# Kernel optimization log

Hardware: AMD Instinct MI355X
Metric: run time of the kernel (lower is better)

The kernel has to match this reference:

```python
import jax, jax.numpy as jnp
import numpy as np
from jax import lax

EPS = 1e-5

def binarize(x):
    # sign forward, straight-through (identity) backward, matching torch .data-trick Binarize
    return x + lax.stop_gradient(jnp.sign(x) - x)

def conv2d(x, w, pad):
    return lax.conv_general_dilated(x, w, window_strides=(1, 1),
                                    padding=[(pad, pad), (pad, pad)],
                                    dimension_numbers=('NCHW', 'OIHW', 'NCHW'))

def maxpool_k2s1(x):
    return lax.reduce_window(x, -jnp.inf, lax.max, (1, 1, 2, 2), (1, 1, 1, 1), 'VALID')

def batchnorm(x, g, b):
    # training-mode BN: batch statistics over (N, H, W)
    mean = jnp.mean(x, axis=(0, 2, 3), keepdims=True)
    var = jnp.var(x, axis=(0, 2, 3), keepdims=True)
    return (x - mean) * lax.rsqrt(var + EPS) * g[None, :, None, None] + b[None, :, None, None]

def hardtanh(x):
    return jnp.clip(x, -1.0, 1.0)

def setup_inputs() -> dict:
    key = jax.random.key(0)
    ks = jax.random.split(key, 11)
    B = 4096
    return {
        'x':   jax.random.normal(ks[0], (B, 12, 12, 15), jnp.float32),
        'w1':  jax.random.normal(ks[1], (48, 12, 3, 3), jnp.float32) * 0.1,
        'g1':  1.0 + 0.1 * jax.random.normal(ks[2], (48,), jnp.float32),
        'b1':  0.1 * jax.random.normal(ks[3], (48,), jnp.float32),
        'w2':  jax.random.normal(ks[4], (48, 48, 3, 3), jnp.float32) * 0.1,
        'g2':  1.0 + 0.1 * jax.random.normal(ks[5], (48,), jnp.float32),
        'b2':  0.1 * jax.random.normal(ks[6], (48,), jnp.float32),
        'w3':  jax.random.normal(ks[7], (48, 48, 3, 3), jnp.float32) * 0.1,
        'g3':  1.0 + 0.1 * jax.random.normal(ks[8], (48,), jnp.float32),
        'b3':  0.1 * jax.random.normal(ks[9], (48,), jnp.float32),
        'wfc': jax.random.normal(ks[10], (5, 54 * 48), jnp.float32) * 0.02,
    }

def reference(x, w1, g1, b1, w2, g2, b2, w3, g3, b3, wfc):
    # BinarizeConv2d binarizes activations (in_channels != 3) and weights; returns binarized input too
    xb1 = binarize(x)                                  # [B,12,12,15]
    h = conv2d(xb1, binarize(w1), pad=1)               # [B,48,12,15]
    h = maxpool_k2s1(h)                                # [B,48,11,14]
    h = hardtanh(batchnorm(h, g1, b1))
    xb2 = binarize(h)
    h = conv2d(xb2, binarize(w2), pad=0)               # [B,48,9,12]
    h = hardtanh(batchnorm(h, g2, b2))
    xb3 = binarize(h)
    h = conv2d(xb3, binarize(w3), pad=0)               # [B,48,7,10]
    h = maxpool_k2s1(h)                                # [B,48,6,9] -> 54 spatial
    h = hardtanh(batchnorm(h, g3, b3))
    f = h.reshape(h.shape[0], -1)                      # [B, 2592]
    fb = binarize(f)
    out = fb @ binarize(wfc).T                         # [B, 5]  (LogSoftmax defined but never applied)
    return (out, xb1, xb2, xb3, fb)
```

## Files before the change

kernel.cpp:

```cpp
#include <hip/hip_runtime.h>
#include <stdint.h>

typedef unsigned long long u64;
typedef unsigned int u32;
typedef unsigned short u16;
typedef unsigned char u8;
typedef signed char s8;

#define NB 4096

#define WS_STATS 0
#define WS_W1Q   20480
#define WS_W2P   24576
#define WS_W3P   28672
#define WS_WFCP  32768
#define WS_A2    40960
#define WS_P1    5087232
#define WS_P3    5087232

#define OUT_OFF 0
#define XB1_OFF 20480
#define XB2_OFF 8867840
#define XB3_OFF 39145472
#define FB_OFF  60379136

__device__ __forceinline__ float fsign(float v) {
    return (v > 0.0f) ? 1.0f : ((v < 0.0f) ? -1.0f : 0.0f);
}
__device__ __forceinline__ int sh16(int v, int h) {
    return h ? (v >> 16) : (int)(short)v;
}

__global__ __launch_bounds__(512)
void kw_pack(const float* __restrict__ w1, const float* __restrict__ w2,
             const float* __restrict__ w3, const float* __restrict__ wfc,
             u32* __restrict__ W1Q, u64* __restrict__ W2P, u64* __restrict__ W3P,
             u64* __restrict__ WFCP, long long* __restrict__ stats) {
    int t = threadIdx.x;
    for (int i = t; i < 2304; i += 512) stats[i] = 0;
    if (t < 48) {
        u16 m1[9];
        #pragma unroll
        for (int p = 0; p < 9; ++p) {
            u16 m = 0;
            for (int c = 0; c < 12; ++c)
                if (w1[t*108 + c*9 + p] > 0.0f) m |= (u16)(1u << c);
            m1[p] = m;
        }
        #pragma unroll
        for (int j = 0; j < 4; ++j)
            W1Q[t*5 + j] = (u32)m1[2*j] | ((u32)m1[2*j+1] << 16);
        W1Q[t*5 + 4] = (u32)m1[8];
    }
    if (t < 432) {
        int oc = t / 9, p = t % 9;
        u64 m2 = 0, m3 = 0;
        for (int c = 0; c < 48; ++c) {
            if (w2[oc*432 + c*9 + p] > 0.0f) m2 |= (1ull << c);
            if (w3[oc*432 + c*9 + p] > 0.0f) m3 |= (1ull << c);
        }
        W2P[t] = m2;
        W3P[t] = m3;
    }
    if (t < 205) {
        int o = t / 41, j = t % 41;
        u64 m = 0;
        for (int l = 0; l < 64; ++l) {
            int k = j*64 + l;
            if (k < 2592 && wfc[o*2592 + k] > 0.0f) m |= (1ull << l);
        }
        WFCP[t] = m;
    }
}

__global__ __launch_bounds__(192)
void k1(const float* __restrict__ x, const u32* __restrict__ W1Q,
        float* __restrict__ dout, u8* __restrict__ P1g, u64* __restrict__ stats) {
    __shared__ u8 bitsb[2160];
    __shared__ u16 As[180];
    __shared__ int cmap[2304];
    __shared__ int2 part[192];
    int t = threadIdx.x, b = blockIdx.x;
    {
        const float4* xp = (const float4*)(x + (size_t)b*2160);
        float4* xo = (float4*)(dout + XB1_OFF + (size_t)b*2160);
        for (int j = t; j < 540; j += 192) {
            float4 v = xp[j];
            float4 o;
            o.x = fsign(v.x); o.y = fsign(v.y); o.z = fsign(v.z); o.w = fsign(v.w);
            xo[j] = o;
            bitsb[4*j]   = v.x > 0.0f;
            bitsb[4*j+1] = v.y > 0.0f;
            bitsb[4*j+2] = v.z > 0.0f;
            bitsb[4*j+3] = v.w > 0.0f;
        }
    }
    __syncthreads();
    if (t < 180) {
        u16 m = 0;
        #pragma unroll
        for (int c = 0; c < 12; ++c)
            m |= ((u16)bitsb[c*180 + t]) << c;
        As[t] = m;
    }
    __syncthreads();
    if (t < 180) {
        int y = t / 15, xx = t % 15;
        u16 tap[9], msk[9];
        int nv = 0;
        #pragma unroll
        for (int ky = 0; ky < 3; ++ky) {
            #pragma unroll
            for (int kx = 0; kx < 3; ++kx) {
                int yy = y + ky - 1, xc = xx + kx - 1;
                bool v = (yy >= 0 && yy < 12 && xc >= 0 && xc < 15);
                int yl = min(max(yy, 0), 11), xl = min(max(xc, 0), 14);
                tap[ky*3+kx] = As[yl*15 + xl];
                msk[ky*3+kx] = v ? (u16)0xFFFF : (u16)0;
                nv += v ? 12 : 0;
            }
        }
        u32 tq[5], mq[5];
        #pragma unroll
        for (int j = 0; j < 4; ++j) {
            tq[j] = (u32)tap[2*j] | ((u32)tap[2*j+1] << 16);
            mq[j] = (u32)msk[2*j] | ((u32)msk[2*j+1] << 16);
        }
        tq[4] = tap[8]; mq[4] = msk[8];
        s8* cb = (s8*)cmap;
        #pragma unroll 4
        for (int oc = 0; oc < 48; ++oc) {
            int acc = 0;
            #pragma unroll
            for (int j = 0; j < 5; ++j)
                acc += __popc((tq[j] ^ W1Q[oc*5 + j]) & mq[j]);
            cb[oc*192 + y*16 + xx] = (s8)(nv - 2*acc);
        }
    }
    __syncthreads();
    {
        int c = t >> 2, q = t & 3;
        int r0 = 3*q, nr = (q < 3) ? 3 : 2;
        int rowv[4][4];
        #pragma unroll
        for (int j = 0; j < 4; ++j)
            if (j <= nr) {
                #pragma unroll
                for (int i = 0; i < 4; ++i)
                    rowv[j][i] = cmap[c*48 + (r0 + j)*4 + i];
            }
        int sum = 0, sq = 0;
        u8* gp = P1g + (size_t)b*8448 + c*176;
        #pragma unroll
        for (int pr = 0; pr < 3; ++pr) {
            if (pr < nr) {
                int o0 = 0, o1 = 0, o2 = 0, o3 = 0;
                #pragma unroll
                for (int k = 0; k < 14; ++k) {
                    int a0 = (int)(s8)(rowv[pr][k>>2] >> (8*(k&3)));
                    int a1 = (int)(s8)(rowv[pr][(k+1)>>2] >> (8*((k+1)&3)));
                    int b0 = (int)(s8)(rowv[pr+1][k>>2] >> (8*(k&3)));
                    int b1 = (int)(s8)(rowv[pr+1][(k+1)>>2] >> (8*((k+1)&3)));
                    int mx = max(max(a0, a1), max(b0, b1));
                    sum += mx; sq += mx*mx;
                    int shl = 8*(k&3);
                    if ((k>>2) == 0) o0 |= (mx & 255) << shl;
                    else if ((k>>2) == 1) o1 |= (mx & 255) << shl;
                    else if ((k>>2) == 2) o2 |= (mx & 255) << shl;
                    else o3 |= (mx & 255) << shl;
                }
                *((int4*)(gp + (r0 + pr)*16)) = make_int4(o0, o1, o2, o3);
            }
        }
        part[t] = make_int2(sum, sq);
    }
    __syncthreads();
    if (t < 48) {
        int s = 0, q = 0;
        #pragma unroll
        for (int k = 0; k < 4; ++k) { s += part[t*4+k].x; q += part[t*4+k].y; }
        int slot = b & 7;
        atomicAdd(&stats[t*8 + slot],        (u64)(long long)s);
        atomicAdd(&stats[(48 + t)*8 + slot], (u64)(long long)q);
    }
}

__global__ __launch_bounds__(256)
void kA(const float* __restrict__ g1, const float* __restrict__ b1,
        const long long* __restrict__ statsIn, const u8* __restrict__ P1g,
        u64* __restrict__ A2, const u64* __restrict__ W2,
        u64* __restrict__ statsOut) {
    __shared__ float sc[48], sh[48];
    __shared__ u64 As[154];
    __shared__ short c2s[5184];
    __shared__ int2 part[192];
    int t = threadIdx.x, b = blockIdx.x;
    if (t < 48) {
        long long s = 0, q = 0;
        #pragma unroll
        for (int k = 0; k < 8; ++k) { s += statsIn[t*8 + k]; q += statsIn[(48 + t)*8 + k]; }
        double N = 630784.0;
        double mean = (double)s / N;
        double var  = (double)q / N - mean*mean;
        double scale = (double)g1[t] / sqrt(var + 1e-5);
        sc[t] = (float)scale;
        sh[t] = (float)((double)b1[t] - mean*scale);
    }
    __syncthreads();
    if (t < 154) {
        int row = t / 14, px = t - 14*row;
        const u8* pb = P1g + (size_t)b*8448 + row*16 + px;
        u64 m = 0;
        #pragma unroll
        for (int c = 0; c < 48; ++c)
            if (sc[c]*(float)(s8)pb[c*176] + sh[c] > 0.0f) m |= (1ull << c);
        As[t] = m;
        A2[(size_t)b*154 + t] = m;
    }
    __syncthreads();
    if (t < 216) {
        int pos = (t < 108) ? t : (t - 108);
        int ocb = (t < 108) ? 0 : 24;
        int oy = pos / 12, ox = pos - 12*oy;
        u64 tap[9];
        #pragma unroll
        for (int ky = 0; ky < 3; ++ky)
            #pragma unroll
            for (int kx = 0; kx < 3; ++kx)
                tap[ky*3+kx] = As[(oy+ky)*14 + ox + kx];
        #pragma unroll 4
        for (int oc = ocb; oc < ocb + 24; ++oc) {
            int acc = 0;
            #pragma unroll
            for (int k = 0; k < 9; ++k)
                acc += __popcll(tap[k] ^ W2[oc*9 + k]);
            c2s[oc*108 + pos] = (short)(432 - 2*acc);
        }
    }
    __syncthreads();
    if (t < 192) {
        int c = t >> 2, q = t & 3;
        const int* ci = (const int*)(c2s + c*108);
        int sum = 0, sq = 0;
        for (int j = q; j < 54; j += 4) {
            int v2 = ci[j];
            int lo = (int)(short)v2, hi = v2 >> 16;
            sum += lo + hi; sq += lo*lo + hi*hi;
        }
        part[t] = make_int2(sum, sq);
    }
    __syncthreads();
    if (t < 48) {
        int s = 0, q = 0;
        #pragma unroll
        for (int k = 0; k < 4; ++k) { s += part[t*4+k].x; q += part[t*4+k].y; }
        int slot = b & 7;
        atomicAdd(&statsOut[(96 + t)*8 + slot],  (u64)(long long)s);
        atomicAdd(&statsOut[(144 + t)*8 + slot], (u64)(long long)q);
    }
}

__global__ __launch_bounds__(256)
void kS2(const float* __restrict__ g1, const float* __restrict__ b1,
         const long long* __restrict__ statsIn, const u8* __restrict__ P1g,
         float* __restrict__ dout) {
    __shared__ float sc[48], sh[48];
    int t = threadIdx.x;
    if (t < 48) {
        long long s = 0, q = 0;
        #pragma unroll
        for (int k = 0; k < 8; ++k) { s += statsIn[t*8 + k]; q += statsIn[(48 + t)*8 + k]; }
        double N = 630784.0;
        double mean = (double)s / N;
        double var  = (double)q / N - mean*mean;
        double scale = (double)g1[t] / sqrt(var + 1e-5);
        sc[t] = (float)scale;
        sh[t] = (float)((double)b1[t] - mean*scale);
    }
    __syncthreads();
    float4* xo = (float4*)(dout + XB2_OFF);
    int gid = blockIdx.x*256 + t;
    for (int j = gid; j < 7569408; j += 1048576) {
        int base = 4*j;
        int b = base / 7392;
        int u = base - 7392*b;
        const u8* pb = P1g + (size_t)b*8448;
        float r[4];
        #pragma unroll
        for (int k = 0; k < 4; ++k) {
            int uk = u + k;
            int c = uk / 154;
            int s = uk - 154*c;
            int row = s / 14;
            int px = s - 14*row;
            int v = (int)(s8)pb[c*176 + row*16 + px];
            r[k] = fsign(sc[c]*(float)v + sh[c]);
        }
        float4 o; o.x = r[0]; o.y = r[1]; o.z = r[2]; o.w = r[3];
        xo[j] = o;
    }
}

__global__ __launch_bounds__(256)
void kB(const float* __restrict__ g2, const float* __restrict__ b2,
        const long long* __restrict__ statsIn, const u64* __restrict__ A2,
        const u64* __restrict__ W2, const u64* __restrict__ W3,
        float* __restrict__ dout, int* __restrict__ P3i,
        u64* __restrict__ statsOut) {
    __shared__ float sc[48], sh[48];
    __shared__ u64 As[154];
    __shared__ short c2s[5184];
    __shared__ u64 A3[108];
    __shared__ short cm[3360];
    __shared__ int2 part[192];
    int t = threadIdx.x, b = blockIdx.x;
    if (t < 154) As[t] = A2[(size_t)b*154 + t];
    if (t < 48) {
        long long s = 0, q = 0;
        #pragma unroll
        for (int k = 0; k < 8; ++k) { s += statsIn[(96 + t)*8 + k]; q += statsIn[(144 + t)*8 + k]; }
        double N = 442368.0;
        double mean = (double)s / N;
        double var  = (double)q / N - mean*mean;
        double scale = (double)g2[t] / sqrt(var + 1e-5);
        sc[t] = (float)scale;
        sh[t] = (float)((double)b2[t] - mean*scale);
    }
    __syncthreads();
    if (t < 216) {
        int pos = (t < 108) ? t : (t - 108);
        int ocb = (t < 108) ? 0 : 24;
        int oy = pos / 12, ox = pos - 12*oy;
        u64 tap[9];
        #pragma unroll
        for (int ky = 0; ky < 3; ++ky)
            #pragma unroll
            for (int kx = 0; kx < 3; ++kx)
                tap[ky*3+kx] = As[(oy+ky)*14 + ox + kx];
        #pragma unroll 4
        for (int oc = ocb; oc < ocb + 24; ++oc) {
            int acc = 0;
            #pragma unroll
            for (int k = 0; k < 9; ++k)
                acc += __popcll(tap[k] ^ W2[oc*9 + k]);
            c2s[oc*108 + pos] = (short)(432 - 2*acc);
        }
    }
    __syncthreads();
    float4* xo = (float4*)(dout + XB3_OFF + (size_t)b*5184);
    for (int i4 = t; i4 < 1296; i4 += 256) {
        int c = i4 / 27, s4 = i4 - 27*c;
        short4 v4 = *(const short4*)&c2s[c*108 + s4*4];
        float4 o;
        o.x = fsign(sc[c]*(float)v4.x + sh[c]);
        o.y = fsign(sc[c]*(float)v4.y + sh[c]);
        o.z = fsign(sc[c]*(float)v4.z + sh[c]);
        o.w = fsign(sc[c]*(float)v4.w + sh[c]);
        xo[i4] = o;
    }
    if (t < 108) {
        u64 m = 0;
        #pragma unroll
        for (int c = 0; c < 48; ++c)
            if (sc[c]*(float)c2s[c*108 + t] + sh[c] > 0.0f) m |= (1ull << c);
        A3[t] = m;
    }
    __syncthreads();
    if (t < 210) {
        int grp = (t < 70) ? 0 : ((t < 140) ? 1 : 2);
        int pos = t - grp*70;
        int ocb = grp*16;
        int oy = pos / 10, ox = pos - 10*oy;
        u64 tap[9];
        #pragma unroll
        for (int ky = 0; ky < 3; ++ky)
            #pragma unroll
            for (int kx = 0; kx < 3; ++kx)
                tap[ky*3+kx] = A3[(oy+ky)*12 + ox + kx];
        #pragma unroll 4
        for (int oc = ocb; oc < ocb + 16; ++oc) {
            int acc = 0;
            #pragma unroll
            for (int k = 0; k < 9; ++k)
                acc += __popcll(tap[k] ^ W3[oc*9 + k]);
            cm[oc*70 + pos] = (short)(432 - 2*acc);
        }
    }
    __syncthreads();
    {
        int c = t >> 2, q = t & 3;
        if (t < 192) {
            int pr0 = (q < 2) ? 2*q : (q + 2);
            int npr = (q < 2) ? 2 : 1;
            int rowv[3][5];
            const int* cmi = (const int*)(cm + c*70);
            #pragma unroll
            for (int j = 0; j < 3; ++j)
                if (j <= npr) {
                    #pragma unroll
                    for (int i = 0; i < 5; ++i)
                        rowv[j][i] = cmi[(pr0 + j)*5 + i];
                }
            int sum = 0, sq = 0;
            int* gp = P3i + (size_t)b*1440 + c*30;
            #pragma unroll
            for (int pr = 0; pr < 2; ++pr) {
                if (pr < npr) {
                    int o[5] = {0, 0, 0, 0, 0};
                    #pragma unroll
                    for (int k = 0; k < 9; ++k) {
                        int a0 = sh16(rowv[pr][k>>1], k&1);
                        int a1 = sh16(rowv[pr][(k+1)>>1], (k+1)&1);
                        int b0 = sh16(rowv[pr+1][k>>1], k&1);
                        int b1 = sh16(rowv[pr+1][(k+1)>>1], (k+1)&1);
                        int mx = max(max(a0, a1), max(b0, b1));
                        sum += mx; sq += mx*mx;
                        o[k>>1] |= (mx & 0xffff) << (16*(k&1));
                    }
                    #pragma unroll
                    for (int j = 0; j < 5; ++j) gp[(pr0 + pr)*5 + j] = o[j];
                }
            }
            part[t] = make_int2(sum, sq);
        }
    }
    __syncthreads();
    if (t < 48) {
        int s = 0, q = 0;
        #pragma unroll
        for (int k = 0; k < 4; ++k) { s += part[t*4+k].x; q += part[t*4+k].y; }
        int slot = b & 7;
        atomicAdd(&statsOut[(192 + t)*8 + slot], (u64)(long long)s);
        atomicAdd(&statsOut[(240 + t)*8 + slot], (u64)(long long)q);
    }
}

__global__ __launch_bounds__(256)
void kC(const float* __restrict__ g3, const float* __restrict__ b3,
        const long long* __restrict__ statsIn, const int4* __restrict__ P3g4,
        const u64* __restrict__ WFC, float* __restrict__ dout) {
    __shared__ float sc[48], sh[48];
    __shared__ int smP[1440];
    __shared__ u8 nib[648];
    __shared__ u64 fbb[41];
    int t = threadIdx.x, b = blockIdx.x;
    for (int i = t; i < 360; i += 256) ((int4*)smP)[i] = P3g4[(size_t)b*360 + i];
    if (t < 48) {
        long long s = 0, q = 0;
        #pragma unroll
        for (int k = 0; k < 8; ++k) { s += statsIn[(192 + t)*8 + k]; q += statsIn[(240 + t)*8 + k]; }
        double N = 221184.0;
        double mean = (double)s / N;
        double var  = (double)q / N - mean*mean;
        double scale = (double)g3[t] / sqrt(var + 1e-5);
        sc[t] = (float)scale;
        sh[t] = (float)((double)b3[t] - mean*scale);
    }
    __syncthreads();
    const short* smS = (const short*)smP;
    float4* fo = (float4*)(dout + FB_OFF + (size_t)b*2592);
    for (int i4 = t; i4 < 648; i4 += 256) {
        int i = 4*i4;
        float r[4];
        unsigned n = 0;
        #pragma unroll
        for (int k = 0; k < 4; ++k) {
            int idx = i + k;
            int c = idx / 54, s = idx - 54*c;
            int row = s / 9, px = s - 9*row;
            float bn = sc[c]*(float)smS[c*60 + row*10 + px] + sh[c];
            r[k] = fsign(bn);
            if (bn > 0.0f) n |= (1u << k);
        }
        float4 o; o.x = r[0]; o.y = r[1]; o.z = r[2]; o.w = r[3];
        fo[i4] = o;
        nib[i4] = (u8)n;
    }
    __syncthreads();
    if (t < 41) {
        u64 m = 0;
        #pragma unroll
        for (int k = 0; k < 16; ++k) {
            int j = t*16 + k;
            if (j < 648) m |= ((u64)nib[j]) << (4*k);
        }
        fbb[t] = m;
    }
    __syncthreads();
    if (t < 5) {
        const u64* Wf = WFC + t*41;
        int acc = 0;
        #pragma unroll
        for (int j = 0; j < 41; ++j) acc += __popcll(fbb[j] ^ Wf[j]);
        dout[OUT_OFF + b*5 + t] = (float)(2592 - 2*acc);
    }
}

extern "C" void kernel_launch(void* const* d_in, const int* in_sizes, int n_in,
                              void* d_out, int out_size, void* d_ws, size_t ws_size,
                              hipStream_t stream) {
    const float* x   = (const float*)d_in[0];
    const float* w1  = (const float*)d_in[1];
    const float* g1  = (const float*)d_in[2];
    const float* b1  = (const float*)d_in[3];
    const float* w2  = (const float*)d_in[4];
    const float* g2  = (const float*)d_in[5];
    const float* b2  = (const float*)d_in[6];
    const float* w3  = (const float*)d_in[7];
    const float* g3  = (const float*)d_in[8];
    const float* b3  = (const float*)d_in[9];
    const float* wfc = (const float*)d_in[10];
    float* out = (float*)d_out;
    char* ws = (char*)d_ws;

    long long* stats = (long long*)(ws + WS_STATS);
    u32*       W1Q   = (u32*)(ws + WS_W1Q);
    u64*       W2P   = (u64*)(ws + WS_W2P);
    u64*       W3P   = (u64*)(ws + WS_W3P);
    u64*       WFCP  = (u64*)(ws + WS_WFCP);
    u64*       A2    = (u64*)(ws + WS_A2);
    u8*        P1g   = (u8*)(ws + WS_P1);
    int*       P3i   = (int*)(ws + WS_P3);

    hipLaunchKernelGGL(kw_pack, dim3(1),    dim3(512), 0, stream,
                       w1, w2, w3, wfc, W1Q, W2P, W3P, WFCP, stats);
    hipLaunchKernelGGL(k1,      dim3(NB),   dim3(192), 0, stream,
                       x, W1Q, out, P1g, (u64*)stats);
    hipLaunchKernelGGL(kA,      dim3(NB),   dim3(256), 0, stream,
                       g1, b1, stats, P1g, A2, W2P, (u64*)stats);
    hipLaunchKernelGGL(kS2,     dim3(NB),   dim3(256), 0, stream,
                       g1, b1, stats, P1g, out);
    hipLaunchKernelGGL(kB,      dim3(NB),   dim3(256), 0, stream,
                       g2, b2, stats, A2, W2P, W3P, out, P3i, (u64*)stats);
    hipLaunchKernelGGL(kC,      dim3(NB),   dim3(256), 0, stream,
                       g3, b3, stats, (const int4*)P3i, WFCP, out);
}
```

Baseline: 641.9 us.

## Fuse all stages into one persistent cooperative kernel with grid syncs

Replaces the six separate kernel launches (weight packing, conv1, BN1/conv2 stats, sign output, conv2/conv3, FC) with a single persistent cooperative kernel. Stages are separated by grid.sync and each block loops over batch items. The kS2 sign-output work is merged into the conv2-stats stage, so P1 is read once there instead of in two kernels. This removes launch gaps and per-kernel tail effects, at the cost of grid-wide barriers and a grid limited to 1024 blocks, which may reduce latency hiding.

```diff
diff --git a/kernel.cpp b/kernel.cpp
--- a/kernel.cpp
+++ b/kernel.cpp
@@ -1,13 +1,14 @@
 #include <hip/hip_runtime.h>
+#include <hip/hip_cooperative_groups.h>
 #include <stdint.h>
+
+namespace cg = cooperative_groups;
 
 typedef unsigned long long u64;
 typedef unsigned int u32;
 typedef unsigned short u16;
 typedef unsigned char u8;
 typedef signed char s8;
-
-#define NB 4096
 
 #define WS_STATS 0
 #define WS_W1Q   20480
@@ -16,7 +17,6 @@
 #define WS_WFCP  32768
 #define WS_A2    40960
 #define WS_P1    5087232
-#define WS_P3    5087232
 
 #define OUT_OFF 0
 #define XB1_OFF 20480
@@ -31,468 +31,456 @@
     return h ? (v >> 16) : (int)(short)v;
 }
 
-__global__ __launch_bounds__(512)
-void kw_pack(const float* __restrict__ w1, const float* __restrict__ w2,
-             const float* __restrict__ w3, const float* __restrict__ wfc,
-             u32* __restrict__ W1Q, u64* __restrict__ W2P, u64* __restrict__ W3P,
-             u64* __restrict__ WFCP, long long* __restrict__ stats) {
-    int t = threadIdx.x;
-    for (int i = t; i < 2304; i += 512) stats[i] = 0;
-    if (t < 48) {
-        u16 m1[9];
-        #pragma unroll
-        for (int p = 0; p < 9; ++p) {
-            u16 m = 0;
-            for (int c = 0; c < 12; ++c)
-                if (w1[t*108 + c*9 + p] > 0.0f) m |= (u16)(1u << c);
-            m1[p] = m;
-        }
-        #pragma unroll
-        for (int j = 0; j < 4; ++j)
-            W1Q[t*5 + j] = (u32)m1[2*j] | ((u32)m1[2*j+1] << 16);
-        W1Q[t*5 + 4] = (u32)m1[8];
+__global__ __launch_bounds__(256, 4)
+void kfull(const float* __restrict__ x,
+           const float* __restrict__ w1, const float* __restrict__ g1, const float* __restrict__ b1,
+           const float* __restrict__ w2, const float* __restrict__ g2, const float* __restrict__ b2,
+           const float* __restrict__ w3, const float* __restrict__ g3, const float* __restrict__ b3,
+           const float* __restrict__ wfc,
+           float* __restrict__ dout,
+           long long* __restrict__ stats,
+           u32* __restrict__ W1Q, u64* __restrict__ W2P, u64* __restrict__ W3P,
+           u64* __restrict__ WFCP, u64* __restrict__ A2,
+           u8* P1g, int* P3i) {
+    cg::grid_group grid = cg::this_grid();
+    __shared__ char smem[21632];
+    int2*  part = (int2*)smem;
+    float* sc   = (float*)(smem + 2048);
+    float* sh   = (float*)(smem + 2240);
+    int t = threadIdx.x, blk = blockIdx.x;
+    int nblk = gridDim.x;
+
+    if (blk == 0) {
+        if (t < 48) {
+            u16 m1[9];
+            #pragma unroll
+            for (int p = 0; p < 9; ++p) {
+                u16 m = 0;
+                for (int c = 0; c < 12; ++c)
+                    if (w1[t*108 + c*9 + p] > 0.0f) m |= (u16)(1u << c);
+                m1[p] = m;
+            }
+            #pragma unroll
+            for (int j = 0; j < 4; ++j)
+                W1Q[t*5 + j] = (u32)m1[2*j] | ((u32)m1[2*j+1] << 16);
+            W1Q[t*5 + 4] = (u32)m1[8];
+        }
+        for (int i = t; i < 432; i += 256) {
+            int oc = i / 9, p = i % 9;
+            u64 m2 = 0, m3 = 0;
+            for (int c = 0; c < 48; ++c) {
+                if (w2[oc*432 + c*9 + p] > 0.0f) m2 |= (1ull << c);
+                if (w3[oc*432 + c*9 + p] > 0.0f) m3 |= (1ull << c);
+            }
+            W2P[i] = m2;
+            W3P[i] = m3;
+        }
+        for (int i = t; i < 205; i += 256) {
+            int o = i / 41, j = i % 41;
+            u64 m = 0;
+            for (int l = 0; l < 64; ++l) {
+                int k = j*64 + l;
+                if (k < 2592 && wfc[o*2592 + k] > 0.0f) m |= (1ull << l);
+            }
+            WFCP[i] = m;
+        }
+    } else if (blk == 1) {
+        for (int i = t; i < 2304; i += 256) stats[i] = 0;
     }
-    if (t < 432) {
-        int oc = t / 9, p = t % 9;
-        u64 m2 = 0, m3 = 0;
-        for (int c = 0; c < 48; ++c) {
-            if (w2[oc*432 + c*9 + p] > 0.0f) m2 |= (1ull << c);
-            if (w3[oc*432 + c*9 + p] > 0.0f) m3 |= (1ull << c);
-        }
-        W2P[t] = m2;
-        W3P[t] = m3;
+    __threadfence();
+    grid.sync();
+
+    {
+        u8*  bitsb = (u8*)(smem + 2432);
+        u16* As1   = (u16*)(smem + 4608);
+        int* cmap  = (int*)(smem + 4976);
+        for (int b = blk; b < 4096; b += nblk) {
+            const float4* xp = (const float4*)(x + (size_t)b*2160);
+            float4* xo = (float4*)(dout + XB1_OFF + (size_t)b*2160);
+            for (int j = t; j < 540; j += 256) {
+                float4 v = xp[j];
+                float4 o;
+                o.x = fsign(v.x); o.y = fsign(v.y); o.z = fsign(v.z); o.w = fsign(v.w);
+                xo[j] = o;
+                bitsb[4*j]   = v.x > 0.0f;
+                bitsb[4*j+1] = v.y > 0.0f;
+                bitsb[4*j+2] = v.z > 0.0f;
+                bitsb[4*j+3] = v.w > 0.0f;
+            }
+            __syncthreads();
+            if (t < 180) {
+                u16 m = 0;
+                #pragma unroll
+                for (int c = 0; c < 12; ++c)
+                    m |= ((u16)bitsb[c*180 + t]) << c;
+                As1[t] = m;
+            }
+            __syncthreads();
+            if (t < 180) {
+                int y = t / 15, xx = t % 15;
+                u16 tap[9], msk[9];
+                int nv = 0;
+                #pragma unroll
+                for (int ky = 0; ky < 3; ++ky) {
+                    #pragma unroll
+                    for (int kx = 0; kx < 3; ++kx) {
+                        int yy = y + ky - 1, xc = xx + kx - 1;
+                        bool v = (yy >= 0 && yy < 12 && xc >= 0 && xc < 15);
+                        int yl = min(max(yy, 0), 11), xl = min(max(xc, 0), 14);
+                        tap[ky*3+kx] = As1[yl*15 + xl];
+                        msk[ky*3+kx] = v ? (u16)0xFFFF : (u16)0;
+                        nv += v ? 12 : 0;
+                    }
+                }
+                u32 tq[5], mq[5];
+                #pragma unroll
+                for (int j = 0; j < 4; ++j) {
+                    tq[j] = (u32)tap[2*j] | ((u32)tap[2*j+1] << 16);
+                    mq[j] = (u32)msk[2*j] | ((u32)msk[2*j+1] << 16);
+                }
+                tq[4] = tap[8]; mq[4] = msk[8];
+                s8* cb = (s8*)cmap;
+                #pragma unroll 4
+                for (int oc = 0; oc < 48; ++oc) {
+                    int acc = 0;
+                    #pragma unroll
+                    for (int j = 0; j < 5; ++j)
+                        acc += __popc((tq[j] ^ W1Q[oc*5 + j]) & mq[j]);
+                    cb[oc*192 + y*16 + xx] = (s8)(nv - 2*acc);
+                }
+            }
+            __syncthreads();
+            if (t < 192) {
+                int c = t >> 2, q = t & 3;
+                int r0 = 3*q, nr = (q < 3) ? 3 : 2;
+                int rowv[4][4];
+                #pragma unroll
+                for (int j = 0; j < 4; ++j)
+                    if (j <= nr) {
+                        #pragma unroll
+                        for (int i = 0; i < 4; ++i)
+                            rowv[j][i] = cmap[c*48 + (r0 + j)*4 + i];
+                    }
+                int sum = 0, sq = 0;
+                u8* gp = P1g + (size_t)b*8448 + c*176;
+                #pragma unroll
+                for (int pr = 0; pr < 3; ++pr) {
+                    if (pr < nr) {
+                        int o0 = 0, o1 = 0, o2 = 0, o3 = 0;
+                        #pragma unroll
+                        for (int k = 0; k < 14; ++k) {
+                            int a0 = (int)(s8)(rowv[pr][k>>2] >> (8*(k&3)));
+                            int a1 = (int)(s8)(rowv[pr][(k+1)>>2] >> (8*((k+1)&3)));
+                            int b0 = (int)(s8)(rowv[pr+1][k>>2] >> (8*(k&3)));
+                            int b1 = (int)(s8)(rowv[pr+1][(k+1)>>2] >> (8*((k+1)&3)));
+                            int mx = max(max(a0, a1), max(b0, b1));
+                            sum += mx; sq += mx*mx;
+                            int shl = 8*(k&3);
+                            if ((k>>2) == 0) o0 |= (mx & 255) << shl;
+                            else if ((k>>2) == 1) o1 |= (mx & 255) << shl;
+                            else if ((k>>2) == 2) o2 |= (mx & 255) << shl;
+                            else o3 |= (mx & 255) << shl;
+                        }
+                        *((int4*)(gp + (r0 + pr)*16)) = make_int4(o0, o1, o2, o3);
+                    }
+                }
+                part[t] = make_int2(sum, sq);
+            }
+            __syncthreads();
+            if (t < 48) {
+                int s = 0, q = 0;
+                #pragma unroll
+                for (int k = 0; k < 4; ++k) { s += part[t*4+k].x; q += part[t*4+k].y; }
+                int slot = b & 7;
+                atomicAdd((u64*)&stats[t*8 + slot],        (u64)(long long)s);
+                atomicAdd((u64*)&stats[(48 + t)*8 + slot], (u64)(long long)q);
+            }
+            __syncthreads();
+        }
     }
-    if (t < 205) {
-        int o = t / 41, j = t % 41;
-        u64 m = 0;
-        for (int l = 0; l < 64; ++l) {
-            int k = j*64 + l;
-            if (k < 2592 && wfc[o*2592 + k] > 0.0f) m |= (1ull << l);
-        }
-        WFCP[t] = m;
+    __threadfence();
+    grid.sync();
+
+    {
+        if (t < 48) {
+            long long s = 0, q = 0;
+            #pragma unroll
+            for (int k = 0; k < 8; ++k) { s += stats[t*8 + k]; q += stats[(48 + t)*8 + k]; }
+            double N = 630784.0;
+            double mean = (double)s / N;
+            double var  = (double)q / N - mean*mean;
+            double scale = (double)g1[t] / sqrt(var + 1e-5);
+            sc[t] = (float)scale;
+            sh[t] = (float)((double)b1[t] - mean*scale);
+        }
+        __syncthreads();
+        u64*   As2 = (u64*)(smem + 2432);
+        short* c2s = (short*)(smem + 3664);
+        for (int b = blk; b < 4096; b += nblk) {
+            const u8* pb = P1g + (size_t)b*8448;
+            float4* xo = (float4*)(dout + XB2_OFF + (size_t)b*7392);
+            for (int i4 = t; i4 < 1848; i4 += 256) {
+                int i = 4*i4;
+                float r[4];
+                #pragma unroll
+                for (int k = 0; k < 4; ++k) {
+                    int uk = i + k;
+                    int c = uk / 154;
+                    int s = uk - 154*c;
+                    int row = s / 14;
+                    int px = s - 14*row;
+                    int v = (int)(s8)pb[c*176 + row*16 + px];
+                    r[k] = fsign(sc[c]*(float)v + sh[c]);
+                }
+                float4 o; o.x = r[0]; o.y = r[1]; o.z = r[2]; o.w = r[3];
+                xo[i4] = o;
+            }
+            if (t < 154) {
+                int row = t / 14, px = t - 14*row;
+                const u8* pbe = pb + row*16 + px;
+                u64 m = 0;
+                #pragma unroll
+                for (int c = 0; c < 48; ++c)
+                    if (sc[c]*(float)(s8)pbe[c*176] + sh[c] > 0.0f) m |= (1ull << c);
+                As2[t] = m;
+                A2[(size_t)b*154 + t] = m;
+            }
+            __syncthreads();
+            if (t < 216) {
+                int pos = (t < 108) ? t : (t - 108);
+                int ocb = (t < 108) ? 0 : 24;
+                int oy = pos / 12, ox = pos - 12*oy;
+                u64 tap[9];
+                #pragma unroll
+                for (int ky = 0; ky < 3; ++ky)
+                    #pragma unroll
+                    for (int kx = 0; kx < 3; ++kx)
+                        tap[ky*3+kx] = As2[(oy+ky)*14 + ox + kx];
+                #pragma unroll 4
+                for (int oc = ocb; oc < ocb + 24; ++oc) {
+                    int acc = 0;
+                    #pragma unroll
+                    for (int k = 0; k < 9; ++k)
+                        acc += __popcll(tap[k] ^ W2P[oc*9 + k]);
+                    c2s[oc*108 + pos] = (short)(432 - 2*acc);
+                }
+            }
+            __syncthreads();
+            if (t < 192) {
+                int c = t >> 2, q = t & 3;
+                const int* ci = (const int*)(c2s + c*108);
+                int sum = 0, sq = 0;
+                for (int j = q; j < 54; j += 4) {
+                    int v2 = ci[j];
+                    int lo = (int)(short)v2, hi = v2 >> 16;
+                    sum += lo + hi; sq += lo*lo + hi*hi;
+                }
+                part[t] = make_int2(sum, sq);
+            }
+            __syncthreads();
+            if (t < 48) {
+                int s = 0, q = 0;
+                #pragma unroll
+                for (int k = 0; k < 4; ++k) { s += part[t*4+k].x; q += part[t*4+k].y; }
+                int slot = b & 7;
+                atomicAdd((u64*)&stats[(96 + t)*8 + slot],  (u64)(long long)s);
+                atomicAdd((u64*)&stats[(144 + t)*8 + slot], (u64)(long long)q);
+            }
+            __syncthreads();
+        }
     }
-}
-
-__global__ __launch_bounds__(192)
-void k1(const float* __restrict__ x, const u32* __restrict__ W1Q,
-        float* __restrict__ dout, u8* __restrict__ P1g, u64* __restrict__ stats) {
-    __shared__ u8 bitsb[2160];
-    __shared__ u16 As[180];
-    __shared__ int cmap[2304];
-    __shared__ int2 part[192];
-    int t = threadIdx.x, b = blockIdx.x;
+    __threadfence();
+    grid.sync();
+
     {
-        const float4* xp = (const float4*)(x + (size_t)b*2160);
-        float4* xo = (float4*)(dout + XB1_OFF + (size_t)b*2160);
-        for (int j = t; j < 540; j += 192) {
-            float4 v = xp[j];
-            float4 o;
-            o.x = fsign(v.x); o.y = fsign(v.y); o.z = fsign(v.z); o.w = fsign(v.w);
-            xo[j] = o;
-            bitsb[4*j]   = v.x > 0.0f;
-            bitsb[4*j+1] = v.y > 0.0f;
-            bitsb[4*j+2] = v.z > 0.0f;
-            bitsb[4*j+3] = v.w > 0.0f;
+        if (t < 48) {
+            long long s = 0, q = 0;
+            #pragma unroll
+            for (int k = 0; k < 8; ++k) { s += stats[(96 + t)*8 + k]; q += stats[(144 + t)*8 + k]; }
+            double N = 442368.0;
+            double mean = (double)s / N;
+            double var  = (double)q / N - mean*mean;
+            double scale = (double)g2[t] / sqrt(var + 1e-5);
+            sc[t] = (float)scale;
+            sh[t] = (float)((double)b2[t] - mean*scale);
+        }
+        __syncthreads();
+        u64*   As2 = (u64*)(smem + 2432);
+        short* c2s = (short*)(smem + 3664);
+        u64*   A3s = (u64*)(smem + 14032);
+        short* cm  = (short*)(smem + 14896);
+        for (int b = blk; b < 4096; b += nblk) {
+            if (t < 154) As2[t] = A2[(size_t)b*154 + t];
+            __syncthreads();
+            if (t < 216) {
+                int pos = (t < 108) ? t : (t - 108);
+                int ocb = (t < 108) ? 0 : 24;
+                int oy = pos / 12, ox = pos - 12*oy;
+                u64 tap[9];
+                #pragma unroll
+                for (int ky = 0; ky < 3; ++ky)
+                    #pragma unroll
+                    for (int kx = 0; kx < 3; ++kx)
+                        tap[ky*3+kx] = As2[(oy+ky)*14 + ox + kx];
+                #pragma unroll 4
+                for (int oc = ocb; oc < ocb + 24; ++oc) {
+                    int acc = 0;
+                    #pragma unroll
+                    for (int k = 0; k < 9; ++k)
+                        acc += __popcll(tap[k] ^ W2P[oc*9 + k]);
+                    c2s[oc*108 + pos] = (short)(432 - 2*acc);
+                }
+            }
+            __syncthreads();
+            float4* xo = (float4*)(dout + XB3_OFF + (size_t)b*5184);
+            for (int i4 = t; i4 < 1296; i4 += 256) {
+                int c = i4 / 27, s4 = i4 - 27*c;
+                short4 v4 = *(const short4*)&c2s[c*108 + s4*4];
+                float4 o;
+                o.x = fsign(sc[c]*(float)v4.x + sh[c]);
+                o.y = fsign(sc[c]*(float)v4.y + sh[c]);
+                o.z = fsign(sc[c]*(float)v4.z + sh[c]);
+                o.w = fsign(sc[c]*(float)v4.w + sh[c]);
+                xo[i4] = o;
+            }
+            if (t < 108) {
+                u64 m = 0;
+                #pragma unroll
+                for (int c = 0; c < 48; ++c)
+                    if (sc[c]*(float)c2s[c*108 + t] + sh[c] > 0.0f) m |= (1ull << c);
+                A3s[t] = m;
+            }
+            __syncthreads();
+            if (t < 210) {
+                int grp = (t < 70) ? 0 : ((t < 140) ? 1 : 2);
+                int pos = t - grp*70;
+                int ocb = grp*16;
+                int oy = pos / 10, ox = pos - 10*oy;
+                u64 tap[9];
+                #pragma unroll
+                for (int ky = 0; ky < 3; ++ky)
+                    #pragma unroll
+                    for (int kx = 0; kx < 3; ++kx)
+                        tap[ky*3+kx] = A3s[(oy+ky)*12 + ox + kx];
+                #pragma unroll 4
+                for (int oc = ocb; oc < ocb + 16; ++oc) {
+                    int acc = 0;
+                    #pragma unroll
+                    for (int k = 0; k < 9; ++k)
+                        acc += __popcll(tap[k] ^ W3P[oc*9 + k]);
+                    cm[oc*70 + pos] = (short)(432 - 2*acc);
+                }
+            }
+            __syncthreads();
+            if (t < 192) {
+                int c = t >> 2, q = t & 3;
+                int pr0 = (q < 2) ? 2*q : (q + 2);
+                int npr = (q < 2) ? 2 : 1;
+                int rowv[3][5];
+                const int* cmi = (const int*)(cm + c*70);
+                #pragma unroll
+                for (int j = 0; j < 3; ++j)
+                    if (j <= npr) {
+                        #pragma unroll
+                        for (int i = 0; i < 5; ++i)
+                            rowv[j][i] = cmi[(pr0 + j)*5 + i];
+                    }
+                int sum = 0, sq = 0;
+                int* gp = P3i + (size_t)b*1440 + c*30;
+                #pragma unroll
+                for (int pr = 0; pr < 2; ++pr) {
+                    if (pr < npr) {
+                        int o[5] = {0, 0, 0, 0, 0};
+                        #pragma unroll
+                        for (int k = 0; k < 9; ++k) {
+                            int a0 = sh16(rowv[pr][k>>1], k&1);
+                            int a1 = sh16(rowv[pr][(k+1)>>1], (k+1)&1);
+                            int b0 = sh16(rowv[pr+1][k>>1], k&1);
+                            int b1 = sh16(rowv[pr+1][(k+1)>>1], (k+1)&1);
+                            int mx = max(max(a0, a1), max(b0, b1));
+                            sum += mx; sq += mx*mx;
+                            o[k>>1] |= (mx & 0xffff) << (16*(k&1));
+                        }
+                        #pragma unroll
+                        for (int j = 0; j < 5; ++j) gp[(pr0 + pr)*5 + j] = o[j];
+                    }
+                }
+                part[t] = make_int2(sum, sq);
+            }
+            __syncthreads();
+            if (t < 48) {
+                int s = 0, q = 0;
+                #pragma unroll
+                for (int k = 0; k < 4; ++k) { s += part[t*4+k].x; q += part[t*4+k].y; }
+                int slot = b & 7;
+                atomicAdd((u64*)&stats[(192 + t)*8 + slot], (u64)(long long)s);
+                atomicAdd((u64*)&stats[(240 + t)*8 + slot], (u64)(long long)q);
+            }
+            __syncthreads();
         }
     }
-    __syncthreads();
-    if (t < 180) {
-        u16 m = 0;
-        #pragma unroll
-        for (int c = 0; c < 12; ++c)
-            m |= ((u16)bitsb[c*180 + t]) << c;
-        As[t] = m;
-    }
-    __syncthreads();
-    if (t < 180) {
-        int y = t / 15, xx = t % 15;
-        u16 tap[9], msk[9];
-        int nv = 0;
-        #pragma unroll
-        for (int ky = 0; ky < 3; ++ky) {
+    __threadfence();
+    grid.sync();
+
+    {
+        if (t < 48) {
+            long long s = 0, q = 0;
             #pragma unroll
-            for (int kx = 0; kx < 3; ++kx) {
-                int yy = y + ky - 1, xc = xx + kx - 1;
-                bool v = (yy >= 0 && yy < 12 && xc >= 0 && xc < 15);
-                int yl = min(max(yy, 0), 11), xl = min(max(xc, 0), 14);
-                tap[ky*3+kx] = As[yl*15 + xl];
-                msk[ky*3+kx] = v ? (u16)0xFFFF : (u16)0;
-                nv += v ? 12 : 0;
-            }
-        }
-        u32 tq[5], mq[5];
-        #pragma unroll
-        for (int j = 0; j < 4; ++j) {
-            tq[j] = (u32)tap[2*j] | ((u32)tap[2*j+1] << 16);
-            mq[j] = (u32)msk[2*j] | ((u32)msk[2*j+1] << 16);
-        }
-        tq[4] = tap[8]; mq[4] = msk[8];
-        s8* cb = (s8*)cmap;
-        #pragma unroll 4
-        for (int oc = 0; oc < 48; ++oc) {
-            int acc = 0;
-            #pragma unroll
-            for (int j = 0; j < 5; ++j)
-                acc += __popc((tq[j] ^ W1Q[oc*5 + j]) & mq[j]);
-            cb[oc*192 + y*16 + xx] = (s8)(nv - 2*acc);
-        }
-    }
-    __syncthreads();
-    {
-        int c = t >> 2, q = t & 3;
-        int r0 = 3*q, nr = (q < 3) ? 3 : 2;
-        int rowv[4][4];
-        #pragma unroll
-        for (int j = 0; j < 4; ++j)
-            if (j <= nr) {
-                #pragma unroll
-                for (int i = 0; i < 4; ++i)
-                    rowv[j][i] = cmap[c*48 + (r0 + j)*4 + i];
-            }
-        int sum = 0, sq = 0;
-        u8* gp = P1g + (size_t)b*8448 + c*176;
-        #pragma unroll
-        for (int pr = 0; pr < 3; ++pr) {
-            if (pr < nr) {
-                int o0 = 0, o1 = 0, o2 = 0, o3 = 0;
-                #pragma unroll
-                for (int k = 0; k < 14; ++k) {
-                    int a0 = (int)(s8)(rowv[pr][k>>2] >> (8*(k&3)));
-                    int a1 = (int)(s8)(rowv[pr][(k+1)>>2] >> (8*((k+1)&3)));
-                    int b0 = (int)(s8)(rowv[pr+1][k>>2] >> (8*(k&3)));
-                    int b1 = (int)(s8)(rowv[pr+1][(k+1)>>2] >> (8*((k+1)&3)));
-                    int mx = max(max(a0, a1), max(b0, b1));
-                    sum += mx; sq += mx*mx;
-                    int shl = 8*(k&3);
-                    if ((k>>2) == 0) o0 |= (mx & 255) << shl;
-                    else if ((k>>2) == 1) o1 |= (mx & 255) << shl;
-                    else if ((k>>2) == 2) o2 |= (mx & 255) << shl;
-                    else o3 |= (mx & 255) << shl;
-                }
-                *((int4*)(gp + (r0 + pr)*16)) = make_int4(o0, o1, o2, o3);
-            }
-        }
-        part[t] = make_int2(sum, sq);
-    }
-    __syncthreads();
-    if (t < 48) {
-        int s = 0, q = 0;
-        #pragma unroll
-        for (int k = 0; k < 4; ++k) { s += part[t*4+k].x; q += part[t*4+k].y; }
-        int slot = b & 7;
-        atomicAdd(&stats[t*8 + slot],        (u64)(long long)s);
-        atomicAdd(&stats[(48 + t)*8 + slot], (u64)(long long)q);
-    }
-}
-
-__global__ __launch_bounds__(256)
-void kA(const float* __restrict__ g1, const float* __restrict__ b1,
-        const long long* __restrict__ statsIn, const u8* __restrict__ P1g,
-        u64* __restrict__ A2, const u64* __restrict__ W2,
-        u64* __restrict__ statsOut) {
-    __shared__ float sc[48], sh[48];
-    __shared__ u64 As[154];
-    __shared__ short c2s[5184];
-    __shared__ int2 part[192];
-    int t = threadIdx.x, b = blockIdx.x;
-    if (t < 48) {
-        long long s = 0, q = 0;
-        #pragma unroll
-        for (int k = 0; k < 8; ++k) { s += statsIn[t*8 + k]; q += statsIn[(48 + t)*8 + k]; }
-        double N = 630784.0;
-        double mean = (double)s / N;
-        double var  = (double)q / N - mean*mean;
-        double scale = (double)g1[t] / sqrt(var + 1e-5);
-        sc[t] = (float)scale;
-        sh[t] = (float)((double)b1[t] - mean*scale);
-    }
-    __syncthreads();
-    if (t < 154) {
-        int row = t / 14, px = t - 14*row;
-        const u8* pb = P1g + (size_t)b*8448 + row*16 + px;
-        u64 m = 0;
-        #pragma unroll
-        for (int c = 0; c < 48; ++c)
-            if (sc[c]*(float)(s8)pb[c*176] + sh[c] > 0.0f) m |= (1ull << c);
-        As[t] = m;
-        A2[(size_t)b*154 + t] = m;
-    }
-    __syncthreads();
-    if (t < 216) {
-        int pos = (t < 108) ? t : (t - 108);
-        int ocb = (t < 108) ? 0 : 24;
-        int oy = pos / 12, ox = pos - 12*oy;
-        u64 tap[9];
-        #pragma unroll
-        for (int ky = 0; ky < 3; ++ky)
-            #pragma unroll
-            for (int kx = 0; kx < 3; ++kx)
-                tap[ky*3+kx] = As[(oy+ky)*14 + ox + kx];
-        #pragma unroll 4
-        for (int oc = ocb; oc < ocb + 24; ++oc) {
-            int acc = 0;
-            #pragma unroll
-            for (int k = 0; k < 9; ++k)
-                acc += __popcll(tap[k] ^ W2[oc*9 + k]);
-            c2s[oc*108 + pos] = (short)(432 - 2*acc);
-        }
-    }
-    __syncthreads();
-    if (t < 192) {
-        int c = t >> 2, q = t & 3;
-        const int* ci = (const int*)(c2s + c*108);
-        int sum = 0, sq = 0;
-        for (int j = q; j < 54; j += 4) {
-            int v2 = ci[j];
-            int lo = (int)(short)v2, hi = v2 >> 16;
-            sum += lo + hi; sq += lo*lo + hi*hi;
-        }
-        part[t] = make_int2(sum, sq);
-    }
-    __syncthreads();
-    if (t < 48) {
-        int s = 0, q = 0;
-        #pragma unroll
-        for (int k = 0; k < 4; ++k) { s += part[t*4+k].x; q += part[t*4+k].y; }
-        int slot = b & 7;
-        atomicAdd(&statsOut[(96 + t)*8 + slot],  (u64)(long long)s);
-        atomicAdd(&statsOut[(144 + t)*8 + slot], (u64)(long long)q);
-    }
-}
-
-__global__ __launch_bounds__(256)
-void kS2(const float* __restrict__ g1, const float* __restrict__ b1,
-         const long long* __restrict__ statsIn, const u8* __restrict__ P1g,
-         float* __restrict__ dout) {
-    __shared__ float sc[48], sh[48];
-    int t = threadIdx.x;
-    if (t < 48) {
-        long long s = 0, q = 0;
-        #pragma unroll
-        for (int k = 0; k < 8; ++k) { s += statsIn[t*8 + k]; q += statsIn[(48 + t)*8 + k]; }
-        double N = 630784.0;
-        double mean = (double)s / N;
-        double var  = (double)q / N - mean*mean;
-        double scale = (double)g1[t] / sqrt(var + 1e-5);
-        sc[t] = (float)scale;
-        sh[t] = (float)((double)b1[t] - mean*scale);
-    }
-    __syncthreads();
-    float4* xo = (float4*)(dout + XB2_OFF);
-    int gid = blockIdx.x*256 + t;
-    for (int j = gid; j < 7569408; j += 1048576) {
-        int base = 4*j;
-        int b = base / 7392;
-        int u = base - 7392*b;
-        const u8* pb = P1g + (size_t)b*8448;
-        float r[4];
-        #pragma unroll
-        for (int k = 0; k < 4; ++k) {
-            int uk = u + k;
-            int c = uk / 154;
-            int s = uk - 154*c;
-            int row = s / 14;
-            int px = s - 14*row;
-            int v = (int)(s8)pb[c*176 + row*16 + px];
-            r[k] = fsign(sc[c]*(float)v + sh[c]);
-        }
-        float4 o; o.x = r[0]; o.y = r[1]; o.z = r[2]; o.w = r[3];
-        xo[j] = o;
-    }
-}
-
-__global__ __launch_bounds__(256)
-void kB(const float* __restrict__ g2, const float* __restrict__ b2,
-        const long long* __restrict__ statsIn, const u64* __restrict__ A2,
-        const u64* __restrict__ W2, const u64* __restrict__ W3,
-        float* __restrict__ dout, int* __restrict__ P3i,
-        u64* __restrict__ statsOut) {
-    __shared__ float sc[48], sh[48];
-    __shared__ u64 As[154];
-    __shared__ short c2s[5184];
-    __shared__ u64 A3[108];
-    __shared__ short cm[3360];
-    __shared__ int2 part[192];
-    int t = threadIdx.x, b = blockIdx.x;
-    if (t < 154) As[t] = A2[(size_t)b*154 + t];
-    if (t < 48) {
-        long long s = 0, q = 0;
-        #pragma unroll
-        for (int k = 0; k < 8; ++k) { s += statsIn[(96 + t)*8 + k]; q += statsIn[(144 + t)*8 + k]; }
-        double N = 442368.0;
-        double mean = (double)s / N;
-        double var  = (double)q / N - mean*mean;
-        double scale = (double)g2[t] / sqrt(var + 1e-5);
-        sc[t] = (float)scale;
-        sh[t] = (float)((double)b2[t] - mean*scale);
-    }
-    __syncthreads();
-    if (t < 216) {
-        int pos = (t < 108) ? t : (t - 108);
-        int ocb = (t < 108) ? 0 : 24;
-        int oy = pos / 12, ox = pos - 12*oy;
-        u64 tap[9];
-        #pragma unroll
-        for (int ky = 0; ky < 3; ++ky)
-            #pragma unroll
-            for (int kx = 0; kx < 3; ++kx)
-                tap[ky*3+kx] = As[(oy+ky)*14 + ox + kx];
-        #pragma unroll 4
-        for (int oc = ocb; oc < ocb + 24; ++oc) {
-            int acc = 0;
-            #pragma unroll
-            for (int k = 0; k < 9; ++k)
-                acc += __popcll(tap[k] ^ W2[oc*9 + k]);
-            c2s[oc*108 + pos] = (short)(432 - 2*acc);
-        }
-    }
-    __syncthreads();
-    float4* xo = (float4*)(dout + XB3_OFF + (size_t)b*5184);
-    for (int i4 = t; i4 < 1296; i4 += 256) {
-        int c = i4 / 27, s4 = i4 - 27*c;
-        short4 v4 = *(const short4*)&c2s[c*108 + s4*4];
-        float4 o;
-        o.x = fsign(sc[c]*(float)v4.x + sh[c]);
-        o.y = fsign(sc[c]*(float)v4.y + sh[c]);
-        o.z = fsign(sc[c]*(float)v4.z + sh[c]);
-        o.w = fsign(sc[c]*(float)v4.w + sh[c]);
-        xo[i4] = o;
-    }
-    if (t < 108) {
-        u64 m = 0;
-        #pragma unroll
-        for (int c = 0; c < 48; ++c)
-            if (sc[c]*(float)c2s[c*108 + t] + sh[c] > 0.0f) m |= (1ull << c);
-        A3[t] = m;
-    }
-    __syncthreads();
-    if (t < 210) {
-        int grp = (t < 70) ? 0 : ((t < 140) ? 1 : 2);
-        int pos = t - grp*70;
-        int ocb = grp*16;
-        int oy = pos / 10, ox = pos - 10*oy;
-        u64 tap[9];
-        #pragma unroll
-        for (int ky = 0; ky < 3; ++ky)
-            #pragma unroll
-            for (int kx = 0; kx < 3; ++kx)
-                tap[ky*3+kx] = A3[(oy+ky)*12 + ox + kx];
-        #pragma unroll 4
-        for (int oc = ocb; oc < ocb + 16; ++oc) {
-            int acc = 0;
-            #pragma unroll
-            for (int k = 0; k < 9; ++k)
-                acc += __popcll(tap[k] ^ W3[oc*9 + k]);
-            cm[oc*70 + pos] = (short)(432 - 2*acc);
-        }
-    }
-    __syncthreads();
-    {
-        int c = t >> 2, q = t & 3;
-        if (t < 192) {
-            int pr0 = (q < 2) ? 2*q : (q + 2);
-            int npr = (q < 2) ? 2 : 1;
-            int rowv[3][5];
-            const int* cmi = (const int*)(cm + c*70);
-            #pragma unroll
-            for (int j = 0; j < 3; ++j)
-                if (j <= npr) {
-                    #pragma unroll
-                    for (int i = 0; i < 5; ++i)
-                        rowv[j][i] = cmi[(pr0 + j)*5 + i];
-                }
-            int sum = 0, sq = 0;
-            int* gp = P3i + (size_t)b*1440 + c*30;
-            #pragma unroll
-            for (int pr = 0; pr < 2; ++pr) {
-                if (pr < npr) {
-                    int o[5] = {0, 0, 0, 0, 0};
-                    #pragma unroll
-                    for (int k = 0; k < 9; ++k) {
-                        int a0 = sh16(rowv[pr][k>>1], k&1);
-                        int a1 = sh16(rowv[pr][(k+1)>>1], (k+1)&1);
-                        int b0 = sh16(rowv[pr+1][k>>1], k&1);
-                        int b1 = sh16(rowv[pr+1][(k+1)>>1], (k+1)&1);
-                        int mx = max(max(a0, a1), max(b0, b1));
-                        sum += mx; sq += mx*mx;
-                        o[k>>1] |= (mx & 0xffff) << (16*(k&1));
-                    }
-                    #pragma unroll
-                    for (int j = 0; j < 5; ++j) gp[(pr0 + pr)*5 + j] = o[j];
-                }
-            }
-            part[t] = make_int2(sum, sq);
-        }
-    }
-    __syncthreads();
-    if (t < 48) {
-        int s = 0, q = 0;
-        #pragma unroll
-        for (int k = 0; k < 4; ++k) { s += part[t*4+k].x; q += part[t*4+k].y; }
-        int slot = b & 7;
-        atomicAdd(&statsOut[(192 + t)*8 + slot], (u64)(long long)s);
-        atomicAdd(&statsOut[(240 + t)*8 + slot], (u64)(long long)q);
-    }
-}
-
-__global__ __launch_bounds__(256)
-void kC(const float* __restrict__ g3, const float* __restrict__ b3,
-        const long long* __restrict__ statsIn, const int4* __restrict__ P3g4,
-        const u64* __restrict__ WFC, float* __restrict__ dout) {
-    __shared__ float sc[48], sh[48];
-    __shared__ int smP[1440];
-    __shared__ u8 nib[648];
-    __shared__ u64 fbb[41];
-    int t = threadIdx.x, b = blockIdx.x;
-    for (int i = t; i < 360; i += 256) ((int4*)smP)[i] = P3g4[(size_t)b*360 + i];
-    if (t < 48) {
-        long long s = 0, q = 0;
-        #pragma unroll
-        for (int k = 0; k < 8; ++k) { s += statsIn[(192 + t)*8 + k]; q += statsIn[(240 + t)*8 + k]; }
-        double N = 221184.0;
-        double mean = (double)s / N;
-        double var  = (double)q / N - mean*mean;
-        double scale = (double)g3[t] / sqrt(var + 1e-5);
-        sc[t] = (float)scale;
-        sh[t] = (float)((double)b3[t] - mean*scale);
-    }
-    __syncthreads();
-    const short* smS = (const short*)smP;
-    float4* fo = (float4*)(dout + FB_OFF + (size_t)b*2592);
-    for (int i4 = t; i4 < 648; i4 += 256) {
-        int i = 4*i4;
-        float r[4];
-        unsigned n = 0;
-        #pragma unroll
-        for (int k = 0; k < 4; ++k) {
-            int idx = i + k;
-            int c = idx / 54, s = idx - 54*c;
-            int row = s / 9, px = s - 9*row;
-            float bn = sc[c]*(float)smS[c*60 + row*10 + px] + sh[c];
-            r[k] = fsign(bn);
-            if (bn > 0.0f) n |= (1u << k);
-        }
-        float4 o; o.x = r[0]; o.y = r[1]; o.z = r[2]; o.w = r[3];
-        fo[i4] = o;
-        nib[i4] = (u8)n;
-    }
-    __syncthreads();
-    if (t < 41) {
-        u64 m = 0;
-        #pragma unroll
-        for (int k = 0; k < 16; ++k) {
-            int j = t*16 + k;
-            if (j < 648) m |= ((u64)nib[j]) << (4*k);
-        }
-        fbb[t] = m;
-    }
-    __syncthreads();
-    if (t < 5) {
-        const u64* Wf = WFC + t*41;
-        int acc = 0;
-        #pragma unroll
-        for (int j = 0; j < 41; ++j) acc += __popcll(fbb[j] ^ Wf[j]);
-        dout[OUT_OFF + b*5 + t] = (float)(2592 - 2*acc);
+            for (int k = 0; k < 8; ++k) { s += stats[(192 + t)*8 + k]; q += stats[(240 + t)*8 + k]; }
+            double N = 221184.0;
+            double mean = (double)s / N;
+            double var  = (double)q / N - mean*mean;
+            double scale = (double)g3[t] / sqrt(var + 1e-5);
+            sc[t] = (float)scale;
+            sh[t] = (float)((double)b3[t] - mean*scale);
+        }
+        __syncthreads();
+        int* smP = (int*)(smem + 2432);
+        u8*  nib = (u8*)(smem + 8192);
+        u64* fbb = (u64*)(smem + 8840);
+        for (int b = blk; b < 4096; b += nblk) {
+            const int4* p4 = (const int4*)(P3i + (size_t)b*1440);
+            for (int i = t; i < 360; i += 256) ((int4*)smP)[i] = p4[i];
+            __syncthreads();
+            const short* smS = (const short*)smP;
+            float4* fo = (float4*)(dout + FB_OFF + (size_t)b*2592);
+            for (int i4 = t; i4 < 648; i4 += 256) {
+                int i = 4*i4;
+                float r[4];
+                unsigned n = 0;
+                #pragma unroll
+                for (int k = 0; k < 4; ++k) {
+                    int idx = i + k;
+                    int c = idx / 54, s = idx - 54*c;
+                    int row = s / 9, px = s - 9*row;
+                    float bn = sc[c]*(float)smS[c*60 + row*10 + px] + sh[c];
+                    r[k] = fsign(bn);
+                    if (bn > 0.0f) n |= (1u << k);
+                }
+                float4 o; o.x = r[0]; o.y = r[1]; o.z = r[2]; o.w = r[3];
+                fo[i4] = o;
+                nib[i4] = (u8)n;
+            }
+            __syncthreads();
+            if (t < 41) {
+                u64 m = 0;
+                #pragma unroll
+                for (int k = 0; k < 16; ++k) {
+                    int j = t*16 + k;
+                    if (j < 648) m |= ((u64)nib[j]) << (4*k);
+                }
+                fbb[t] = m;
+            }
+            __syncthreads();
+            if (t < 5) {
+                const u64* Wf = WFCP + t*41;
+                int acc = 0;
+                #pragma unroll
+                for (int j = 0; j < 41; ++j) acc += __popcll(fbb[j] ^ Wf[j]);
+                dout[OUT_OFF + b*5 + t] = (float)(2592 - 2*acc);
+            }
+            __syncthreads();
+        }
     }
 }
 
@@ -520,18 +508,22 @@
     u64*       WFCP  = (u64*)(ws + WS_WFCP);
     u64*       A2    = (u64*)(ws + WS_A2);
     u8*        P1g   = (u8*)(ws + WS_P1);
-    int*       P3i   = (int*)(ws + WS_P3);
-
-    hipLaunchKernelGGL(kw_pack, dim3(1),    dim3(512), 0, stream,
-                       w1, w2, w3, wfc, W1Q, W2P, W3P, WFCP, stats);
-    hipLaunchKernelGGL(k1,      dim3(NB),   dim3(192), 0, stream,
-                       x, W1Q, out, P1g, (u64*)stats);
-    hipLaunchKernelGGL(kA,      dim3(NB),   dim3(256), 0, stream,
-                       g1, b1, stats, P1g, A2, W2P, (u64*)stats);
-    hipLaunchKernelGGL(kS2,     dim3(NB),   dim3(256), 0, stream,
-                       g1, b1, stats, P1g, out);
-    hipLaunchKernelGGL(kB,      dim3(NB),   dim3(256), 0, stream,
-                       g2, b2, stats, A2, W2P, W3P, out, P3i, (u64*)stats);
-    hipLaunchKernelGGL(kC,      dim3(NB),   dim3(256), 0, stream,
-                       g3, b3, stats, (const int4*)P3i, WFCP, out);
+    int*       P3i   = (int*)(ws + WS_P1);
+
+    int perCU = 0;
+    hipError_t qe = hipOccupancyMaxActiveBlocksPerMultiprocessor(&perCU, kfull, 256, 0);
+    int gridBlocks = (qe == hipSuccess && perCU > 0) ? perCU * 256 : 256;
+    if (gridBlocks > 1024) gridBlocks = 1024;
+    if (gridBlocks < 2)    gridBlocks = 2;
+
+    void* args[] = {
+        (void*)&x, (void*)&w1, (void*)&g1, (void*)&b1,
+        (void*)&w2, (void*)&g2, (void*)&b2,
+        (void*)&w3, (void*)&g3, (void*)&b3,
+        (void*)&wfc, (void*)&out, (void*)&stats,
+        (void*)&W1Q, (void*)&W2P, (void*)&W3P,
+        (void*)&WFCP, (void*)&A2, (void*)&P1g, (void*)&P3i
+    };
+    hipLaunchCooperativeKernel((void*)kfull, dim3(gridBlocks), dim3(256),
+                               args, 0, stream);
 }
```

New measurement: 1.074 ms. +67.2%, slower.
